# Optimization experiments

Hardware: AMD Instinct MI355X
Metric: run time of the kernel (lower is better)

## Reference

```python
import jax, jax.numpy as jnp
import numpy as np

N_NODES = 8192
IN_F = 256
OUT_F = 256
ALPHA = 0.2  # LeakyReLU negative slope


def setup_inputs() -> dict:
    key = jax.random.key(0)
    k1, k2, k3, k4 = jax.random.split(key, 4)
    X = jax.random.normal(k1, (N_NODES, IN_F), dtype=jnp.float32)
    A = jax.random.randint(k2, (N_NODES, N_NODES), 0, 2, dtype=jnp.int32)
    # torch nn.Linear weight layout: (out_features, in_features)
    W = jax.random.normal(k3, (OUT_F, IN_F), dtype=jnp.float32) * (1.0 / np.sqrt(IN_F))
    r = jax.random.normal(k4, (2 * OUT_F, 1), dtype=jnp.float32)
    return {"X": X, "A": A, "W": W, "r": r}


def reference(X, A, W, r):
    # Wh = X @ W^T  -> (N, F_out)
    Wh = X @ W.T
    # Split r so that cat([Wh_i, Wh_j]) @ r == Wh_i @ r_src + Wh_j @ r_dst
    F_out = Wh.shape[-1]
    r_src = r[:F_out, 0]   # (F,)
    r_dst = r[F_out:, 0]   # (F,)
    s_i = Wh @ r_src       # (N,)
    s_j = Wh @ r_dst       # (N,)
    e = s_i[:, None] + s_j[None, :]                      # (N, N)
    e = jnp.where(e >= 0, e, ALPHA * e)                  # LeakyReLU
    e = jnp.where(A == 0, -jnp.inf, e)                   # mask non-edges
    attention = jax.nn.softmax(e, axis=1)                # row-wise softmax
    output = attention @ Wh                              # (N, F_out)
    return jax.nn.gelu(output, approximate=False)        # torch F.gelu (exact)
```

## Files before the change

### kernel.cpp

```cpp
#include <hip/hip_runtime.h>
#include <hip/hip_bf16.h>

#define N_NODES 8192
#define NF      256
#define L2E     1.44269504088896341f

typedef __attribute__((ext_vector_type(8))) short short8;
typedef __attribute__((ext_vector_type(4))) short short4v;
typedef __attribute__((ext_vector_type(4))) float floatx4;
typedef __attribute__((ext_vector_type(16))) float floatx16;

static __device__ __forceinline__ float bf2f(short s) {
    return __uint_as_float(((unsigned)(unsigned short)s) << 16);
}
static __device__ __forceinline__ short f2bf_rn(float f) {
    unsigned u = __float_as_uint(f) + 0x8000u;
    return (short)(u >> 16);
}
struct bfpair { short hi, lo; };
static __device__ __forceinline__ bfpair split_bf(float x) {
    bfpair p;
    p.hi = f2bf_rn(x);
    p.lo = f2bf_rn(x - bf2f(p.hi));
    return p;
}
static __device__ __forceinline__ void async16(const void* g, void* l) {
    __builtin_amdgcn_global_load_lds(
        (const __attribute__((address_space(1))) unsigned*)g,
        (__attribute__((address_space(3))) unsigned*)l, 16, 0, 0);
}

__global__ __launch_bounds__(256) void kx_split(const float* __restrict__ W,
                                                short* __restrict__ Whi,
                                                short* __restrict__ Wlo) {
    #pragma unroll
    for (int e = 0; e < 4; ++e) {
        const int i = blockIdx.x * 1024 + e * 256 + threadIdx.x;
        bfpair p = split_bf(W[i]);
        Whi[i] = p.hi;
        Wlo[i] = p.lo;
    }
}

__global__ __launch_bounds__(512) void k1_gemm(const float* __restrict__ X,
                                               const short* __restrict__ Whi,
                                               const short* __restrict__ Wlo,
                                               const float* __restrict__ r,
                                               short* __restrict__ WhT,
                                               float* __restrict__ sp_src,
                                               float* __restrict__ sp_dst) {
    __shared__ float Xs[32 * 256];

    const int tid = threadIdx.x;
    const int w = tid >> 6, lane = tid & 63;
    const int q = lane >> 4, m = lane & 15;
    const int rh = w >> 2, cq = w & 3;
    const int i_base = blockIdx.x * 32;

    #pragma unroll
    for (int v = 0; v < 4; ++v) {
        const int rowv = w * 4 + v;
        const int c = lane ^ (rowv & 7);
        async16(X + (size_t)(i_base + rowv) * NF + c * 4, &Xs[rowv * 256]);
    }
    __syncthreads();

    floatx4 acc[4] = {};
    const int xrow = rh * 16 + m;
    const int r7 = xrow & 7;
    #pragma unroll
    for (int ks = 0; ks < 8; ++ks) {
        const int c0 = ks * 8 + q * 2;
        float4 f0 = *(const float4*)(&Xs[xrow * 256 + ((c0 ^ r7) * 4)]);
        float4 f1 = *(const float4*)(&Xs[xrow * 256 + (((c0 + 1) ^ r7) * 4)]);
        const float xsv[8] = {f0.x, f0.y, f0.z, f0.w, f1.x, f1.y, f1.z, f1.w};
        short8 xh, xl;
        #pragma unroll
        for (int c = 0; c < 8; ++c) {
            bfpair p = split_bf(xsv[c]);
            xh[c] = p.hi; xl[c] = p.lo;
        }
        #pragma unroll
        for (int nt = 0; nt < 4; ++nt) {
            const int n = cq * 64 + nt * 16 + m;
            short8 wh = *(const short8*)(Whi + n * NF + ks * 32 + q * 8);
            short8 wl = *(const short8*)(Wlo + n * NF + ks * 32 + q * 8);
            acc[nt] = __builtin_amdgcn_mfma_f32_16x16x32_bf16(xh, wh, acc[nt], 0, 0, 0);
            acc[nt] = __builtin_amdgcn_mfma_f32_16x16x32_bf16(xl, wh, acc[nt], 0, 0, 0);
            acc[nt] = __builtin_amdgcn_mfma_f32_16x16x32_bf16(xh, wl, acc[nt], 0, 0, 0);
        }
    }

    const int i0 = i_base + rh * 16 + q * 4;
    float vs[4] = {0.f, 0.f, 0.f, 0.f}, vd[4] = {0.f, 0.f, 0.f, 0.f};
    #pragma unroll
    for (int nt = 0; nt < 4; ++nt) {
        const int n = cq * 64 + nt * 16 + m;
        short4v v;
        #pragma unroll
        for (int r2 = 0; r2 < 4; ++r2) v[r2] = f2bf_rn(acc[nt][r2]);
        *(short4v*)(WhT + (size_t)n * N_NODES + i0) = v;
        const float rs = r[n], rd = r[NF + n];
        #pragma unroll
        for (int r2 = 0; r2 < 4; ++r2) {
            vs[r2] = fmaf(acc[nt][r2], rs, vs[r2]);
            vd[r2] = fmaf(acc[nt][r2], rd, vd[r2]);
        }
    }
    #pragma unroll
    for (int mask = 1; mask <= 8; mask <<= 1) {
        #pragma unroll
        for (int r2 = 0; r2 < 4; ++r2) {
            vs[r2] += __shfl_xor(vs[r2], mask);
            vd[r2] += __shfl_xor(vd[r2], mask);
        }
    }
    if (m == 0) {
        #pragma unroll
        for (int r2 = 0; r2 < 4; ++r2) {
            sp_src[cq * N_NODES + i0 + r2] = vs[r2];
            sp_dst[cq * N_NODES + i0 + r2] = vd[r2];
        }
    }
}

__global__ __launch_bounds__(256) void k2_sv(const float* __restrict__ sp_src,
                                             const float* __restrict__ sp_dst,
                                             float* __restrict__ s_src,
                                             float* __restrict__ s_dst,
                                             float* __restrict__ pmax) {
    __shared__ float red[256];
    const int tid = threadIdx.x;
    const int i = blockIdx.x * 256 + tid;
    float ss = 0.f, sd = 0.f;
    #pragma unroll
    for (int nb = 0; nb < 4; ++nb) {
        ss += sp_src[nb * N_NODES + i];
        sd += sp_dst[nb * N_NODES + i];
    }
    s_src[i] = ss;
    s_dst[i] = sd;
    red[tid] = sd;
    __syncthreads();
    for (int off = 128; off > 0; off >>= 1) {
        if (tid < off) red[tid] = fmaxf(red[tid], red[tid + off]);
        __syncthreads();
    }
    if (tid == 0) pmax[blockIdx.x] = red[0];
}

static __device__ __forceinline__ void pgroup(const int4 a, const floatx4 t,
                                              const float s_i, const float d_i,
                                              float* p) {
    const int av[4] = {a.x, a.y, a.z, a.w};
    #pragma unroll
    for (int c = 0; c < 4; ++c) {
        float sum = s_i + t[c];
        float lr  = fmaxf(sum, 0.2f * sum);
        float pp  = __builtin_amdgcn_exp2f(fmaf(lr, L2E, d_i));
        p[c] = (av[c] != 0) ? pp : 0.0f;
    }
}

__global__ __launch_bounds__(512, 4) void k4_attn(const int* __restrict__ Adj,
                                                  const short* __restrict__ WhT,
                                                  const float* __restrict__ s_dst,
                                                  const float* __restrict__ s_src,
                                                  const float* __restrict__ pmax,
                                                  float* __restrict__ nump,
                                                  float* __restrict__ denp) {
    __shared__ union {
        short B[2][256 * 64];
        float red[8 * 16 * 64];
    } sm;
    __shared__ float denred[4 * 32];

    const int tid = threadIdx.x;
    const int w = tid >> 6, lane = tid & 63;
    const int jq = w & 3, nh = w >> 2;
    const int l31 = lane & 31, lh = lane >> 5;
    const int ib = (int)blockIdx.x >> 1, jh = (int)blockIdx.x & 1;
    const int i0 = ib * 32;
    const int row = i0 + l31;
    const int jbase = jh * 4096;

    float M = pmax[0];
    #pragma unroll
    for (int b = 1; b < 32; ++b) M = fmaxf(M, pmax[b]);
    const float s_i = s_src[row];
    const float e0 = s_i + M;
    const float d_i = -fmaxf(e0, 0.2f * e0) * L2E;

    int voff[4];
    #pragma unroll
    for (int v = 0; v < 4; ++v) {
        const int rown = w * 32 + v * 8 + (lane >> 3);
        const int c = (lane & 7) ^ (rown & 7);
        voff[v] = rown * N_NODES + c * 8;
    }
    const short* gBbase = WhT + jbase;

    const int g = jq * 2 + lh;
    int boff[4];
    #pragma unroll
    for (int nt = 0; nt < 4; ++nt) {
        const int n = nh * 128 + nt * 32 + l31;
        boff[nt] = n * 64 + ((g ^ (l31 & 7)) * 8);
    }

    const int j0 = jq * 16 + lh * 8;
    const int* aPtr = Adj + (size_t)row * N_NODES + jbase + j0;
    const float* tPtr = s_dst + jbase + j0;

    floatx16 acc[4] = {};
    float den = 0.f;

    #pragma unroll
    for (int v = 0; v < 4; ++v)
        async16(gBbase + voff[v], &sm.B[0][(w * 32 + v * 8) * 64]);
    int4 a0 = *(const int4*)(aPtr);
    int4 a1 = *(const int4*)(aPtr + 4);
    __syncthreads();

    for (int s = 0; s < 64; ++s) {
        const short* Bc = sm.B[s & 1];
        short* Bn = sm.B[(s & 1) ^ 1];

        if (s < 63) {
            const int jo = (s + 1) * 64;
            #pragma unroll
            for (int v = 0; v < 4; ++v)
                async16(gBbase + jo + voff[v], Bn + (w * 32 + v * 8) * 64);
        }
        const int an = (s < 63) ? (s + 1) * 64 : s * 64;
        int4 na0 = *(const int4*)(aPtr + an);
        int4 na1 = *(const int4*)(aPtr + an + 4);
        const float* tp = tPtr + s * 64;
        floatx4 t0 = *(const floatx4*)(tp);
        floatx4 t1 = *(const floatx4*)(tp + 4);

        float p[8];
        pgroup(a0, t0, s_i, d_i, p);
        pgroup(a1, t1, s_i, d_i, p + 4);

        short8 af;
        float ds = 0.f;
        #pragma unroll
        for (int c = 0; c < 8; ++c) { af[c] = f2bf_rn(p[c]); ds += p[c]; }
        den += ds;

        #pragma unroll
        for (int nt = 0; nt < 4; ++nt) {
            short8 b = *(const short8*)(Bc + boff[nt]);
            acc[nt] = __builtin_amdgcn_mfma_f32_32x32x16_bf16(af, b, acc[nt], 0, 0, 0);
        }
        a0 = na0; a1 = na1;

        __syncthreads();
    }

    den += __shfl_xor(den, 32);
    if (w < 4 && lane < 32) denred[w * 32 + lane] = den;

    float* numq = nump + (size_t)jh * N_NODES * NF;
    #pragma unroll
    for (int nt = 0; nt < 4; ++nt) {
        #pragma unroll
        for (int rg = 0; rg < 16; ++rg)
            sm.red[(w * 16 + rg) * 64 + lane] = acc[nt][rg];
        __syncthreads();
        if (nt == 0 && tid < 32) {
            float d = denred[tid] + denred[32 + tid] + denred[64 + tid] + denred[96 + tid];
            denp[jh * N_NODES + i0 + tid] = d;
        }
        const int nh2 = w & 1;
        const int rb = (w >> 1) * 4;
        #pragma unroll
        for (int k = 0; k < 4; ++k) {
            const int rg = rb + k;
            float v = sm.red[((nh2 * 4 + 0) * 16 + rg) * 64 + lane]
                    + sm.red[((nh2 * 4 + 1) * 16 + rg) * 64 + lane]
                    + sm.red[((nh2 * 4 + 2) * 16 + rg) * 64 + lane]
                    + sm.red[((nh2 * 4 + 3) * 16 + rg) * 64 + lane];
            const int rrow = (rg & 3) + 8 * (rg >> 2) + 4 * lh;
            const int nn = nh2 * 128 + nt * 32 + l31;
            numq[(size_t)(i0 + rrow) * NF + nn] = v;
        }
        __syncthreads();
    }
}

__global__ __launch_bounds__(256) void k5_out(const float* __restrict__ nump,
                                              const float* __restrict__ denp,
                                              float* __restrict__ out) {
    const int idx = blockIdx.x * 256 + threadIdx.x;
    const int i = idx >> 8;
    float num = nump[idx] + nump[N_NODES * NF + idx];
    float den = denp[i] + denp[N_NODES + i];
    float x = num / fmaxf(den, 1e-30f);
    out[idx] = 0.5f * x * (1.0f + erff(x * 0.70710678118f));
}

extern "C" void kernel_launch(void* const* d_in, const int* in_sizes, int n_in,
                              void* d_out, int out_size, void* d_ws, size_t ws_size,
                              hipStream_t stream) {
    const float* X = (const float*)d_in[0];
    const int*   A = (const int*)d_in[1];
    const float* W = (const float*)d_in[2];
    const float* r = (const float*)d_in[3];
    float* out = (float*)d_out;

    char* wsp = (char*)d_ws;
    short* WhT    = (short*)wsp;                    wsp += (size_t)NF * N_NODES * 2;
    short* Whi    = (short*)wsp;                    wsp += NF * NF * 2;
    short* Wlo    = (short*)wsp;                    wsp += NF * NF * 2;
    float* sp_src = (float*)wsp;                    wsp += 4 * N_NODES * 4;
    float* sp_dst = (float*)wsp;                    wsp += 4 * N_NODES * 4;
    float* s_src  = (float*)wsp;                    wsp += N_NODES * 4;
    float* s_dst  = (float*)wsp;                    wsp += N_NODES * 4;
    float* pmax   = (float*)wsp;                    wsp += 32 * 4;
    float* denp   = (float*)wsp;                    wsp += 2 * N_NODES * 4;
    float* nump   = (float*)wsp;

    kx_split<<<64, 256, 0, stream>>>(W, Whi, Wlo);
    k1_gemm<<<256, 512, 0, stream>>>(X, Whi, Wlo, r, WhT, sp_src, sp_dst);
    k2_sv<<<32, 256, 0, stream>>>(sp_src, sp_dst, s_src, s_dst, pmax);
    k4_attn<<<512, 512, 0, stream>>>(A, WhT, s_dst, s_src, pmax, nump, denp);
    k5_out<<<N_NODES * NF / 256, 256, 0, stream>>>(nump, denp, out);
}
```

Measured before the change: 488.2 us.

## Pack adjacency into bitmask in a separate pass and split attention blocks by feature half

A new pre-pass reads the int32 adjacency matrix once and packs it into a bitmask. The attention kernel then reads compact bits instead of int32 values. The attention kernel is also restructured to 256-thread blocks, each handling half the output features, with twice as many blocks. The packed mask can be reused by both feature halves, but the full 256MB adjacency is still read once in the pack pass, and the WhT tiles now get loaded per feature half.

```diff
diff --git a/kernel.cpp b/kernel.cpp
--- a/kernel.cpp
+++ b/kernel.cpp
@@ -149,20 +149,50 @@
     if (tid == 0) pmax[blockIdx.x] = red[0];
 }
 
-static __device__ __forceinline__ void pgroup(const int4 a, const floatx4 t,
-                                              const float s_i, const float d_i,
-                                              float* p) {
-    const int av[4] = {a.x, a.y, a.z, a.w};
+__global__ __launch_bounds__(256) void k3_pack(const int* __restrict__ Adj,
+                                               unsigned char* __restrict__ Apk) {
+    const int gid = blockIdx.x * 4 + (threadIdx.x >> 6);
+    const int lane = threadIdx.x & 63;
+    const int row = gid >> 1, jh = gid & 1;
+    const int* base = Adj + (size_t)row * N_NODES + jh * 4096;
+
+    unsigned long long accw = 0;
+    #pragma unroll 4
+    for (int it = 0; it < 64; ++it) {
+        int v = base[it * 64 + lane];
+        unsigned long long m = __ballot(v != 0);
+        if (lane < 8) {
+            unsigned long long byte = (m >> (lane * 8)) & 0xFFull;
+            accw |= byte << ((it & 7) * 8);
+            if ((it & 7) == 7) {
+                *(unsigned long long*)(Apk + (size_t)row * 1024 + jh * 512 +
+                                       lane * 64 + (it & ~7)) = accw;
+                accw = 0;
+            }
+        }
+    }
+}
+
+static __device__ __forceinline__ void pgroup8(unsigned ab, const floatx4 t0,
+                                               const floatx4 t1, const float s_i,
+                                               const float d_i, float* p) {
     #pragma unroll
     for (int c = 0; c < 4; ++c) {
-        float sum = s_i + t[c];
+        float sum = s_i + t0[c];
         float lr  = fmaxf(sum, 0.2f * sum);
         float pp  = __builtin_amdgcn_exp2f(fmaf(lr, L2E, d_i));
-        p[c] = (av[c] != 0) ? pp : 0.0f;
-    }
-}
-
-__global__ __launch_bounds__(512, 4) void k4_attn(const int* __restrict__ Adj,
+        p[c] = (ab & (1u << c)) ? pp : 0.0f;
+    }
+    #pragma unroll
+    for (int c = 0; c < 4; ++c) {
+        float sum = s_i + t1[c];
+        float lr  = fmaxf(sum, 0.2f * sum);
+        float pp  = __builtin_amdgcn_exp2f(fmaf(lr, L2E, d_i));
+        p[4 + c] = (ab & (1u << (4 + c))) ? pp : 0.0f;
+    }
+}
+
+__global__ __launch_bounds__(256, 4) void k4_attn(const unsigned char* __restrict__ Apk,
                                                   const short* __restrict__ WhT,
                                                   const float* __restrict__ s_dst,
                                                   const float* __restrict__ s_src,
@@ -170,16 +200,17 @@
                                                   float* __restrict__ nump,
                                                   float* __restrict__ denp) {
     __shared__ union {
-        short B[2][256 * 64];
-        float red[8 * 16 * 64];
+        short B[2][128 * 64];
+        float red[4 * 16 * 64];
     } sm;
     __shared__ float denred[4 * 32];
 
     const int tid = threadIdx.x;
     const int w = tid >> 6, lane = tid & 63;
-    const int jq = w & 3, nh = w >> 2;
+    const int jq = w;
     const int l31 = lane & 31, lh = lane >> 5;
-    const int ib = (int)blockIdx.x >> 1, jh = (int)blockIdx.x & 1;
+    const int bid = (int)blockIdx.x;
+    const int ib = bid >> 2, jh = (bid >> 1) & 1, nhf = bid & 1;
     const int i0 = ib * 32;
     const int row = i0 + l31;
     const int jbase = jh * 4096;
@@ -194,23 +225,22 @@
     int voff[4];
     #pragma unroll
     for (int v = 0; v < 4; ++v) {
-        const int rown = w * 32 + v * 8 + (lane >> 3);
-        const int c = (lane & 7) ^ (rown & 7);
-        voff[v] = rown * N_NODES + c * 8;
-    }
-    const short* gBbase = WhT + jbase;
+        const int rn = w * 32 + v * 8 + (lane >> 3);
+        const int c = (lane & 7) ^ (rn & 7);
+        voff[v] = rn * N_NODES + c * 8;
+    }
+    const short* gBbase = WhT + (size_t)(nhf * 128) * N_NODES + jbase;
 
     const int g = jq * 2 + lh;
     int boff[4];
     #pragma unroll
     for (int nt = 0; nt < 4; ++nt) {
-        const int n = nh * 128 + nt * 32 + l31;
-        boff[nt] = n * 64 + ((g ^ (l31 & 7)) * 8);
-    }
-
-    const int j0 = jq * 16 + lh * 8;
-    const int* aPtr = Adj + (size_t)row * N_NODES + jbase + j0;
-    const float* tPtr = s_dst + jbase + j0;
+        const int n = nt * 32 + l31;
+        boff[nt] = n * 64 + ((g ^ (n & 7)) * 8);
+    }
+
+    const unsigned char* aRow = Apk + (size_t)row * 1024 + jh * 512 + g * 64;
+    const float* tPtr = s_dst + jbase + g * 8;
 
     floatx16 acc[4] = {};
     float den = 0.f;
@@ -218,49 +248,50 @@
     #pragma unroll
     for (int v = 0; v < 4; ++v)
         async16(gBbase + voff[v], &sm.B[0][(w * 32 + v * 8) * 64]);
-    int4 a0 = *(const int4*)(aPtr);
-    int4 a1 = *(const int4*)(aPtr + 4);
+    unsigned long long abits = *(const unsigned long long*)(aRow);
     __syncthreads();
 
-    for (int s = 0; s < 64; ++s) {
-        const short* Bc = sm.B[s & 1];
-        short* Bn = sm.B[(s & 1) ^ 1];
-
-        if (s < 63) {
-            const int jo = (s + 1) * 64;
+    for (int s8 = 0; s8 < 8; ++s8) {
+        unsigned long long nabits = (s8 < 7)
+            ? *(const unsigned long long*)(aRow + (s8 + 1) * 8) : 0ull;
+        #pragma unroll
+        for (int si = 0; si < 8; ++si) {
+            const int s = s8 * 8 + si;
+            const short* Bc = sm.B[s & 1];
+            short* Bn = sm.B[(s & 1) ^ 1];
+
+            if (s < 63) {
+                const int jo = (s + 1) * 64;
+                #pragma unroll
+                for (int v = 0; v < 4; ++v)
+                    async16(gBbase + jo + voff[v], Bn + (w * 32 + v * 8) * 64);
+            }
+            const unsigned ab = (unsigned)((abits >> (si * 8)) & 0xFFull);
+            const float* tp = tPtr + s * 64;
+            floatx4 t0 = *(const floatx4*)(tp);
+            floatx4 t1 = *(const floatx4*)(tp + 4);
+
+            float p[8];
+            pgroup8(ab, t0, t1, s_i, d_i, p);
+
+            short8 af;
+            float ds = 0.f;
             #pragma unroll
-            for (int v = 0; v < 4; ++v)
-                async16(gBbase + jo + voff[v], Bn + (w * 32 + v * 8) * 64);
-        }
-        const int an = (s < 63) ? (s + 1) * 64 : s * 64;
-        int4 na0 = *(const int4*)(aPtr + an);
-        int4 na1 = *(const int4*)(aPtr + an + 4);
-        const float* tp = tPtr + s * 64;
-        floatx4 t0 = *(const floatx4*)(tp);
-        floatx4 t1 = *(const floatx4*)(tp + 4);
-
-        float p[8];
-        pgroup(a0, t0, s_i, d_i, p);
-        pgroup(a1, t1, s_i, d_i, p + 4);
-
-        short8 af;
-        float ds = 0.f;
-        #pragma unroll
-        for (int c = 0; c < 8; ++c) { af[c] = f2bf_rn(p[c]); ds += p[c]; }
-        den += ds;
-
-        #pragma unroll
-        for (int nt = 0; nt < 4; ++nt) {
-            short8 b = *(const short8*)(Bc + boff[nt]);
-            acc[nt] = __builtin_amdgcn_mfma_f32_32x32x16_bf16(af, b, acc[nt], 0, 0, 0);
-        }
-        a0 = na0; a1 = na1;
-
-        __syncthreads();
+            for (int c = 0; c < 8; ++c) { af[c] = f2bf_rn(p[c]); ds += p[c]; }
+            den += ds;
+
+            #pragma unroll
+            for (int nt = 0; nt < 4; ++nt) {
+                short8 b = *(const short8*)(Bc + boff[nt]);
+                acc[nt] = __builtin_amdgcn_mfma_f32_32x32x16_bf16(af, b, acc[nt], 0, 0, 0);
+            }
+            __syncthreads();
+        }
+        abits = nabits;
     }
 
     den += __shfl_xor(den, 32);
-    if (w < 4 && lane < 32) denred[w * 32 + lane] = den;
+    if (lane < 32) denred[w * 32 + lane] = den;
 
     float* numq = nump + (size_t)jh * N_NODES * NF;
     #pragma unroll
@@ -269,21 +300,19 @@
         for (int rg = 0; rg < 16; ++rg)
             sm.red[(w * 16 + rg) * 64 + lane] = acc[nt][rg];
         __syncthreads();
-        if (nt == 0 && tid < 32) {
+        if (nt == 0 && nhf == 0 && tid < 32) {
             float d = denred[tid] + denred[32 + tid] + denred[64 + tid] + denred[96 + tid];
             denp[jh * N_NODES + i0 + tid] = d;
         }
-        const int nh2 = w & 1;
-        const int rb = (w >> 1) * 4;
         #pragma unroll
         for (int k = 0; k < 4; ++k) {
-            const int rg = rb + k;
-            float v = sm.red[((nh2 * 4 + 0) * 16 + rg) * 64 + lane]
-                    + sm.red[((nh2 * 4 + 1) * 16 + rg) * 64 + lane]
-                    + sm.red[((nh2 * 4 + 2) * 16 + rg) * 64 + lane]
-                    + sm.red[((nh2 * 4 + 3) * 16 + rg) * 64 + lane];
+            const int rg = w * 4 + k;
+            float v = sm.red[((0 * 16) + rg) * 64 + lane]
+                    + sm.red[((1 * 16) + rg) * 64 + lane]
+                    + sm.red[((2 * 16) + rg) * 64 + lane]
+                    + sm.red[((3 * 16) + rg) * 64 + lane];
             const int rrow = (rg & 3) + 8 * (rg >> 2) + 4 * lh;
-            const int nn = nh2 * 128 + nt * 32 + l31;
+            const int nn = nhf * 128 + nt * 32 + l31;
             numq[(size_t)(i0 + rrow) * NF + nn] = v;
         }
         __syncthreads();
@@ -320,11 +349,13 @@
     float* s_dst  = (float*)wsp;                    wsp += N_NODES * 4;
     float* pmax   = (float*)wsp;                    wsp += 32 * 4;
     float* denp   = (float*)wsp;                    wsp += 2 * N_NODES * 4;
-    float* nump   = (float*)wsp;
+    float* nump   = (float*)wsp;                    wsp += (size_t)2 * N_NODES * NF * 4;
+    unsigned char* Apk = (unsigned char*)wsp;
 
     kx_split<<<64, 256, 0, stream>>>(W, Whi, Wlo);
     k1_gemm<<<256, 512, 0, stream>>>(X, Whi, Wlo, r, WhT, sp_src, sp_dst);
     k2_sv<<<32, 256, 0, stream>>>(sp_src, sp_dst, s_src, s_dst, pmax);
-    k4_attn<<<512, 512, 0, stream>>>(A, WhT, s_dst, s_src, pmax, nump, denp);
+    k3_pack<<<4096, 256, 0, stream>>>(A, Apk);
+    k4_attn<<<1024, 256, 0, stream>>>(Apk, WhT, s_dst, s_src, pmax, nump, denp);
     k5_out<<<N_NODES * NF / 256, 256, 0, stream>>>(nump, denp, out);
 }
```

After: 562.5 us. +15.2%, slower.
